# Kernel tuning notes

Hardware: AMD Instinct MI355X
Metric: run time of the kernel (lower is better)

The kernel has to match this reference:

```python
import jax, jax.numpy as jnp
import numpy as np

T, LQ, C = 6, 300, 256
NH, NL, PC, TW, PT = 8, 4, 4, 2, 2
DFF = 1024
HD = C // NH
SHAPES = [(96, 128), (48, 64), (24, 32), (12, 16)]
LIN = sum(h * w for h, w in SHAPES)
EPS = 1e-5


def _ln(x, g, b):
    m = x.mean(-1, keepdims=True)
    v = ((x - m) ** 2).mean(-1, keepdims=True)
    return (x - m) * jax.lax.rsqrt(v + EPS) * g + b


def _bilinear(img, loc):
    # img [T, Hl, Wl, NH, HD]; loc [T, Q, NH, P, 2] (x, y), normalized [0,1],
    # grid_sample align_corners=False + zero padding convention.
    Hl, Wl = img.shape[1], img.shape[2]
    x = loc[..., 0] * Wl - 0.5
    y = loc[..., 1] * Hl - 0.5
    x0f = jnp.floor(x)
    y0f = jnp.floor(y)
    wx = x - x0f
    wy = y - y0f
    x0 = x0f.astype(jnp.int32)
    y0 = y0f.astype(jnp.int32)
    flat = img.transpose(0, 3, 1, 2, 4).reshape(img.shape[0], NH, Hl * Wl, HD)
    b = jnp.arange(img.shape[0])[:, None, None, None]
    h = jnp.arange(NH)[None, :, None, None]

    def corner(yi, xi, w):
        valid = (xi >= 0) & (xi < Wl) & (yi >= 0) & (yi < Hl)
        idx = jnp.clip(yi, 0, Hl - 1) * Wl + jnp.clip(xi, 0, Wl - 1)
        g = flat[b, h, idx.transpose(0, 2, 1, 3)]  # [T, NH, Q, P, HD]
        w = jnp.where(valid, w, 0.0).transpose(0, 2, 1, 3)
        return g * w[..., None]

    out = (corner(y0, x0, (1 - wx) * (1 - wy)) + corner(y0, x0 + 1, wx * (1 - wy))
           + corner(y0 + 1, x0, (1 - wx) * wy) + corner(y0 + 1, x0 + 1, wx * wy))
    return out.transpose(0, 2, 1, 3, 4)  # [T, Q, NH, P, HD]


def _forward(tgt, query_pos, reference_points, curr_frame_offsets,
             other_frames_temporal_offsets, src, src_padding_mask,
             in_proj_w, in_proj_b, sa_out_w, sa_out_b,
             norm1_g, norm1_b, norm2_g, norm2_b, norm3_g, norm3_b,
             value_w, value_b, soff_w, soff_b, toff_w, toff_b,
             attn_w, attn_b, cross_out_w, cross_out_b,
             lin1_w, lin1_b, lin2_w, lin2_b):
    # ---- self attention (per-frame MHA over queries) ----
    q = tgt + query_pos
    wq, wk, wv = jnp.split(in_proj_w, 3, axis=0)
    bq, bk, bv = jnp.split(in_proj_b, 3)
    qh = ((q @ wq.T + bq) * (1.0 / np.sqrt(HD))).reshape(T, LQ, NH, HD)
    kh = (q @ wk.T + bk).reshape(T, LQ, NH, HD)
    vh = (tgt @ wv.T + bv).reshape(T, LQ, NH, HD)
    att = jax.nn.softmax(jnp.einsum('bqhd,bkhd->bhqk', qh, kh), axis=-1)
    sa = jnp.einsum('bhqk,bkhd->bqhd', att, vh).reshape(T, LQ, C) @ sa_out_w.T + sa_out_b
    tgt = _ln(tgt + sa, norm2_g, norm2_b)

    # ---- temporal multi-scale deformable cross attention ----
    qc = tgt + query_pos
    value = src @ value_w.T + value_b
    value = jnp.where(src_padding_mask[..., None], 0.0, value)
    value = value.reshape(T, LIN, NH, HD)

    soff = (qc @ soff_w.T + soff_b).reshape(T, LQ, NH, NL, PC, 2)
    toff = (qc @ toff_w.T + toff_b).reshape(T, LQ, NH, NL, TW, PT, 2)
    aw = (qc @ attn_w.T + attn_b).reshape(T, LQ, NH, NL * (PC + TW * PT))
    aw = jax.nn.softmax(aw, axis=-1).reshape(T, LQ, NH, NL, PC + TW * PT)
    aw_c = aw[..., :PC]                                  # [T,LQ,NH,NL,PC]
    aw_t = aw[..., PC:].reshape(T, LQ, NH, NL, TW, PT)

    norm = jnp.array([[w, h] for h, w in SHAPES], jnp.float32)  # [NL,2] (x,y)
    ref = reference_points[:, :, None, :, None, :]       # [T,LQ,1,NL,1,2]
    cfo = curr_frame_offsets[:, :, None, :, None, :]
    loc_c = ref + cfo + soff / norm[None, None, None, :, None, :]
    ofo = other_frames_temporal_offsets.transpose(0, 1, 3, 2, 4)[:, :, None, :, :, None, :]
    loc_t = ref[:, :, :, :, None, :, :] + ofo + toff / norm[None, None, None, :, None, None, :]

    # temporal window frame indices: nearest neighbours, clipped to clip bounds
    deltas = np.array([-(i // 2 + 1) if i % 2 == 0 else (i // 2 + 1) for i in range(TW)])
    frame_idx = np.clip(np.arange(T)[:, None] + deltas[None, :], 0, T - 1)  # [T,TW]

    out = jnp.zeros((T, LQ, NH, HD), tgt.dtype)
    start = 0
    for l, (hl, wl) in enumerate(SHAPES):
        v_l = value[:, start:start + hl * wl].reshape(T, hl, wl, NH, HD)
        s = _bilinear(v_l, loc_c[:, :, :, l])            # [T,LQ,NH,PC,HD]
        out = out + (s * aw_c[:, :, :, l, :, None]).sum(3)
        for w in range(TW):
            s = _bilinear(v_l[frame_idx[:, w]], loc_t[:, :, :, l, w])
            out = out + (s * aw_t[:, :, :, l, w, :, None]).sum(3)
        start += hl * wl
    cross = out.reshape(T, LQ, C) @ cross_out_w.T + cross_out_b
    tgt = _ln(tgt + cross, norm1_g, norm1_b)

    # ---- FFN ----
    ff = jax.nn.relu(tgt @ lin1_w.T + lin1_b) @ lin2_w.T + lin2_b
    return _ln(tgt + ff, norm3_g, norm3_b)


def setup_inputs():
    ks = jax.random.split(jax.random.key(0), 24)
    r = lambda i, s: jax.random.normal(ks[i], s, jnp.float32)
    u = lambda i, s: jax.random.uniform(ks[i], s, dtype=jnp.float32)
    w = lambda i, s: r(i, s) * 0.02
    shp = np.array(SHAPES, np.int64)
    lsi = np.concatenate([[0], np.cumsum(shp[:, 0] * shp[:, 1])[:-1]])
    return {
        'tgt': r(0, (T, LQ, C)),
        'query_pos': r(1, (T, LQ, C)),
        'reference_points': u(2, (T, LQ, NL, 2)),
        'curr_frame_offsets': u(3, (T, LQ, NL, 2)) * 0.1,
        'other_frames_temporal_offsets': u(4, (T, LQ, TW, NL, 2)) * 0.1,
        'src': r(5, (T, LIN, C)),
        'src_spatial_shapes': jnp.asarray(shp),
        'level_start_index': jnp.asarray(lsi),
        'src_padding_mask': jnp.zeros((T, LIN), bool),
        'in_proj_w': w(6, (3 * C, C)), 'in_proj_b': jnp.zeros((3 * C,)),
        'sa_out_w': w(7, (C, C)), 'sa_out_b': jnp.zeros((C,)),
        'norm1_g': jnp.ones((C,)), 'norm1_b': jnp.zeros((C,)),
        'norm2_g': jnp.ones((C,)), 'norm2_b': jnp.zeros((C,)),
        'norm3_g': jnp.ones((C,)), 'norm3_b': jnp.zeros((C,)),
        'value_w': w(8, (C, C)), 'value_b': jnp.zeros((C,)),
        'soff_w': w(9, (NH * NL * PC * 2, C)), 'soff_b': jnp.zeros((NH * NL * PC * 2,)),
        'toff_w': w(10, (NH * NL * TW * PT * 2, C)), 'toff_b': jnp.zeros((NH * NL * TW * PT * 2,)),
        'attn_w': w(11, (NH * NL * (PC + TW * PT), C)), 'attn_b': jnp.zeros((NH * NL * (PC + TW * PT),)),
        'cross_out_w': w(12, (C, C)), 'cross_out_b': jnp.zeros((C,)),
        'lin1_w': w(13, (DFF, C)), 'lin1_b': jnp.zeros((DFF,)),
        'lin2_w': w(14, (C, DFF)), 'lin2_b': jnp.zeros((C,)),
    }


def reference(tgt, query_pos, reference_points, curr_frame_offsets,
              other_frames_temporal_offsets, src, src_spatial_shapes,
              level_start_index, src_padding_mask,
              in_proj_w, in_proj_b, sa_out_w, sa_out_b,
              norm1_g, norm1_b, norm2_g, norm2_b, norm3_g, norm3_b,
              value_w, value_b, soff_w, soff_b, toff_w, toff_b,
              attn_w, attn_b, cross_out_w, cross_out_b,
              lin1_w, lin1_b, lin2_w, lin2_b):
    # src_spatial_shapes / level_start_index are static (match SHAPES constants)
    return _forward(tgt, query_pos, reference_points, curr_frame_offsets,
                    other_frames_temporal_offsets, src, src_padding_mask,
                    in_proj_w, in_proj_b, sa_out_w, sa_out_b,
                    norm1_g, norm1_b, norm2_g, norm2_b, norm3_g, norm3_b,
                    value_w, value_b, soff_w, soff_b, toff_w, toff_b,
                    attn_w, attn_b, cross_out_w, cross_out_b,
                    lin1_w, lin1_b, lin2_w, lin2_b)
```

## Files before the change

### kernel.cpp

```cpp
#include <hip/hip_runtime.h>
#include <hip/hip_bf16.h>
#include <math.h>

#define T_ 6
#define LQ_ 300
#define C_ 256
#define NH_ 8
#define HD_ 32
#define DFF_ 1024
#define LIN_ 16320
#define NQ_ (T_*LQ_)

typedef unsigned int uint32;
typedef unsigned short us;

__device__ __forceinline__ float b2f(us u) {
    union { float f; unsigned i; } x; x.i = ((unsigned)u) << 16; return x.f;
}
__device__ __forceinline__ us f2b(float f) {
    union { float f; unsigned i; } x; x.f = f;
    unsigned r = x.i + 0x7fffu + ((x.i >> 16) & 1u);
    return (us)(r >> 16);
}
__device__ __forceinline__ uint32 pack2(float a, float b) {
    union { __hip_bfloat162 h; uint32 u; } c;
    c.h = __float22bfloat162_rn(make_float2(a, b));
    return c.u;
}

typedef __bf16 bf16x8 __attribute__((ext_vector_type(8)));
typedef float  f32x4  __attribute__((ext_vector_type(4)));

__device__ __forceinline__ void gemm64_core(
        us* As, us* Bs, int bm,
        const float* __restrict__ A, const float* __restrict__ A2,
        const float* __restrict__ Bw,
        const float* __restrict__ bias, float* __restrict__ Cmat,
        int ldc, int cn0, int M, int K, bool relu) {
    constexpr int LDA = 40;
    int tid  = threadIdx.x;
    int wave = tid >> 6, lane = tid & 63;
    int wm = (wave >> 1) * 32, wn = (wave & 1) * 32;

    f32x4 acc00 = {0.f,0.f,0.f,0.f}, acc01 = {0.f,0.f,0.f,0.f};
    f32x4 acc10 = {0.f,0.f,0.f,0.f}, acc11 = {0.f,0.f,0.f,0.f};

    int srow = tid >> 2, scol = (tid & 3) * 8;
    int arow = bm + srow;
    const bool aval = arow < M;
    const size_t aoff = (size_t)arow * K + scol;
    const size_t boff = (size_t)srow * K + scol;

    int fr = lane & 15, quad = lane >> 4;
    const us* pa0 = As + (wm + fr) * LDA + quad * 8;
    const us* pa1 = pa0 + 16 * LDA;
    const us* pb0 = Bs + (wn + fr) * LDA + quad * 8;
    const us* pb1 = pb0 + 16 * LDA;

    for (int k0 = 0; k0 < K; k0 += 256) {
        float4 ar[8][2], br[8][2];
        #pragma unroll
        for (int c = 0; c < 8; ++c) {
            int kk = k0 + c * 32;
            if (aval) {
                ar[c][0] = *(const float4*)(A + aoff + kk);
                ar[c][1] = *(const float4*)(A + aoff + kk + 4);
                if (A2) {
                    float4 p0 = *(const float4*)(A2 + aoff + kk);
                    float4 p1 = *(const float4*)(A2 + aoff + kk + 4);
                    ar[c][0].x += p0.x; ar[c][0].y += p0.y; ar[c][0].z += p0.z; ar[c][0].w += p0.w;
                    ar[c][1].x += p1.x; ar[c][1].y += p1.y; ar[c][1].z += p1.z; ar[c][1].w += p1.w;
                }
            } else {
                ar[c][0] = make_float4(0.f,0.f,0.f,0.f);
                ar[c][1] = make_float4(0.f,0.f,0.f,0.f);
            }
            br[c][0] = *(const float4*)(Bw + boff + kk);
            br[c][1] = *(const float4*)(Bw + boff + kk + 4);
        }
        #pragma unroll
        for (int c = 0; c < 8; ++c) {
            uint4 ap, bp;
            ap.x = pack2(ar[c][0].x, ar[c][0].y); ap.y = pack2(ar[c][0].z, ar[c][0].w);
            ap.z = pack2(ar[c][1].x, ar[c][1].y); ap.w = pack2(ar[c][1].z, ar[c][1].w);
            bp.x = pack2(br[c][0].x, br[c][0].y); bp.y = pack2(br[c][0].z, br[c][0].w);
            bp.z = pack2(br[c][1].x, br[c][1].y); bp.w = pack2(br[c][1].z, br[c][1].w);
            __syncthreads();
            *(uint4*)(As + srow * LDA + scol) = ap;
            *(uint4*)(Bs + srow * LDA + scol) = bp;
            __syncthreads();
            bf16x8 a0 = *(const bf16x8*)pa0;
            bf16x8 a1 = *(const bf16x8*)pa1;
            bf16x8 b0 = *(const bf16x8*)pb0;
            bf16x8 b1 = *(const bf16x8*)pb1;
            acc00 = __builtin_amdgcn_mfma_f32_16x16x32_bf16(a0, b0, acc00, 0, 0, 0);
            acc01 = __builtin_amdgcn_mfma_f32_16x16x32_bf16(a0, b1, acc01, 0, 0, 0);
            acc10 = __builtin_amdgcn_mfma_f32_16x16x32_bf16(a1, b0, acc10, 0, 0, 0);
            acc11 = __builtin_amdgcn_mfma_f32_16x16x32_bf16(a1, b1, acc11, 0, 0, 0);
        }
    }

    int n0l = wn + fr, n1l = n0l + 16;
    float bias0 = bias[n0l], bias1 = bias[n1l];
    int mbase = bm + wm + quad * 4;
    #pragma unroll
    for (int r = 0; r < 4; ++r) {
        int m0 = mbase + r, m1 = m0 + 16;
        float v00 = acc00[r] + bias0, v01 = acc01[r] + bias1;
        float v10 = acc10[r] + bias0, v11 = acc11[r] + bias1;
        if (relu) {
            v00 = fmaxf(v00, 0.f); v01 = fmaxf(v01, 0.f);
            v10 = fmaxf(v10, 0.f); v11 = fmaxf(v11, 0.f);
        }
        if (m0 < M) {
            Cmat[(size_t)m0 * ldc + cn0 + n0l] = v00;
            Cmat[(size_t)m0 * ldc + cn0 + n1l] = v01;
        }
        if (m1 < M) {
            Cmat[(size_t)m1 * ldc + cn0 + n0l] = v10;
            Cmat[(size_t)m1 * ldc + cn0 + n1l] = v11;
        }
    }
}

template<bool RELU>
__global__ __launch_bounds__(256, 2) void gemm_std(
        const float* __restrict__ A, const float* __restrict__ W,
        const float* __restrict__ bias, float* __restrict__ C,
        int M, int N, int K) {
    __shared__ __align__(16) us As[64 * 40];
    __shared__ __align__(16) us Bs[64 * 40];
    int cn0 = blockIdx.y * 64;
    gemm64_core(As, Bs, blockIdx.x * 64, A, nullptr, W + (size_t)cn0 * K, bias + cn0,
                C, N, cn0, M, K, RELU);
}

__global__ __launch_bounds__(256, 2) void gemm_proj3(
        const float* __restrict__ qc,
        const float* __restrict__ sw, const float* __restrict__ sb,
        const float* __restrict__ tw, const float* __restrict__ tb,
        const float* __restrict__ aw, const float* __restrict__ ab,
        float* __restrict__ so, float* __restrict__ to, float* __restrict__ ao) {
    __shared__ __align__(16) us As[64 * 40];
    __shared__ __align__(16) us Bs[64 * 40];
    int y = blockIdx.y, g = y >> 2, cn0 = (y & 3) * 64;
    const float* W; const float* bias; float* O;
    if (g == 0)      { W = sw; bias = sb; O = so; }
    else if (g == 1) { W = tw; bias = tb; O = to; }
    else             { W = aw; bias = ab; O = ao; }
    gemm64_core(As, Bs, blockIdx.x * 64, qc, nullptr, W + (size_t)cn0 * 256, bias + cn0,
                O, 256, cn0, NQ_, 256, false);
}

__global__ __launch_bounds__(256, 2) void vqkv_kernel(
        const float* __restrict__ src, const float* __restrict__ val_w,
        const float* __restrict__ val_b, us* __restrict__ value,
        const float* __restrict__ tgt, const float* __restrict__ qpos,
        const float* __restrict__ in_w, const float* __restrict__ in_b,
        float* __restrict__ qkb, float* __restrict__ vbuf) {
    __shared__ __align__(16) char smem[32768];
    if (blockIdx.x >= 1530) {
        us* As64 = (us*)smem;
        us* Bs64 = (us*)(smem + 5120);
        int u = blockIdx.x - 1530, y = u / 29, bm = (u % 29) * 64;
        if (y < 8)
            gemm64_core(As64, Bs64, bm, tgt, qpos, in_w + (size_t)y * 64 * 256,
                        in_b + y * 64, qkb, 512, y * 64, NQ_, 256, false);
        else
            gemm64_core(As64, Bs64, bm, tgt, nullptr,
                        in_w + (size_t)(512 + (y - 8) * 64) * 256,
                        in_b + 512 + (y - 8) * 64, vbuf, 256, (y - 8) * 64,
                        NQ_, 256, false);
        return;
    }
    constexpr int LDA = 40;
    us* As = (us*)smem;
    us* Bs = (us*)(smem + 5120);
    int tid = threadIdx.x, wave = tid >> 6, lane = tid & 63;
    int bm = blockIdx.x * 64;
    int fr = lane & 15, quad = lane >> 4;

    f32x4 acc[4][4];
    #pragma unroll
    for (int i = 0; i < 4; ++i)
        #pragma unroll
        for (int j = 0; j < 4; ++j) { f32x4 z = {0.f,0.f,0.f,0.f}; acc[i][j] = z; }

    float4 av[2], bv[8];
    auto ldA = [&](int c) {
        int k0 = c * 32;
        #pragma unroll
        for (int i = 0; i < 2; ++i) {
            int f = i * 256 + tid;
            av[i] = *(const float4*)(src + (size_t)(bm + (f >> 3)) * 256 + k0 + (f & 7) * 4);
        }
    };
    auto ldB = [&](int c) {
        int k0 = c * 32;
        #pragma unroll
        for (int i = 0; i < 8; ++i) {
            int f = i * 256 + tid;
            bv[i] = *(const float4*)(val_w + (size_t)(f >> 3) * 256 + k0 + (f & 7) * 4);
        }
    };

    ldA(0); ldB(0);
    for (int c = 0; c < 8; ++c) {
        if (c) __syncthreads();
        #pragma unroll
        for (int i = 0; i < 2; ++i) {
            int f = i * 256 + tid;
            uint2 p; p.x = pack2(av[i].x, av[i].y); p.y = pack2(av[i].z, av[i].w);
            *(uint2*)(As + (f >> 3) * LDA + (f & 7) * 4) = p;
        }
        #pragma unroll
        for (int i = 0; i < 8; ++i) {
            int f = i * 256 + tid;
            uint2 p; p.x = pack2(bv[i].x, bv[i].y); p.y = pack2(bv[i].z, bv[i].w);
            *(uint2*)(Bs + (f >> 3) * LDA + (f & 7) * 4) = p;
        }
        __syncthreads();
        if (c + 1 < 8) { ldA(c + 1); ldB(c + 1); }
        bf16x8 af[4], bfv[4];
        #pragma unroll
        for (int mt = 0; mt < 4; ++mt)
            af[mt] = *(const bf16x8*)(As + (mt * 16 + fr) * LDA + quad * 8);
        #pragma unroll
        for (int nt = 0; nt < 4; ++nt)
            bfv[nt] = *(const bf16x8*)(Bs + (wave * 64 + nt * 16 + fr) * LDA + quad * 8);
        #pragma unroll
        for (int mt = 0; mt < 4; ++mt)
            #pragma unroll
            for (int nt = 0; nt < 4; ++nt)
                acc[mt][nt] = __builtin_amdgcn_mfma_f32_16x16x32_bf16(af[mt], bfv[nt], acc[mt][nt], 0, 0, 0);
    }

    __syncthreads();
    us* Cs = (us*)smem;
    #pragma unroll
    for (int nt = 0; nt < 4; ++nt) {
        int n = wave * 64 + nt * 16 + fr;
        float bs = val_b[n];
        #pragma unroll
        for (int mt = 0; mt < 4; ++mt) {
            int rowb = mt * 16 + quad * 4;
            #pragma unroll
            for (int r = 0; r < 4; ++r)
                Cs[(rowb + r) * 256 + n] = f2b(acc[mt][nt][r] + bs);
        }
    }
    __syncthreads();
    #pragma unroll
    for (int p = 0; p < 4; ++p) {
        int flat = p * 256 + tid;
        int row = flat >> 5, c16 = (flat & 31) * 8;
        uint4 v = *(const uint4*)(Cs + row * 256 + c16);
        *(uint4*)(value + (size_t)(bm + row) * 256 + c16) = v;
    }
}

__global__ __launch_bounds__(256) void attn_kernel(
        const float* __restrict__ qk, const float* __restrict__ vb,
        float* __restrict__ sain) {
    __shared__ uint32 Ksu[300 * 17];
    __shared__ uint32 Vsu[300 * 17];
    __shared__ float  Qs[32 * 32];
    __shared__ float  ps[4][304];
    int t = blockIdx.x / NH_, h = blockIdx.x % NH_;
    int q0 = blockIdx.y * 32;
    int tid = threadIdx.x;

    for (int idx = tid; idx < 300 * 16; idx += 256) {
        int row = idx >> 4, cc = idx & 15;
        float2 kv = *(const float2*)(qk + (size_t)(t * 300 + row) * 512 + 256 + h * 32 + 2 * cc);
        float2 vv = *(const float2*)(vb + (size_t)(t * 300 + row) * 256 + h * 32 + 2 * cc);
        Ksu[row * 17 + cc] = pack2(kv.x, kv.y);
        Vsu[row * 17 + cc] = pack2(vv.x, vv.y);
    }
    for (int idx = tid; idx < 1024; idx += 256) {
        int row = idx >> 5, d = idx & 31;
        int q = q0 + row;
        Qs[idx] = (q < 300) ? qk[(size_t)(t * 300 + q) * 512 + h * 32 + d] : 0.f;
    }
    __syncthreads();

    int wavei = tid >> 6, lane = tid & 63;
    const float scale = 0.17677669529663687f;

    for (int i = 0; i < 8; ++i) {
        int q = q0 + wavei * 8 + i;
        int ql = wavei * 8 + i;
        float qv[32];
        #pragma unroll
        for (int d = 0; d < 32; ++d) qv[d] = Qs[ql * 32 + d];

        float sc[5], mx = -1e30f;
        #pragma unroll
        for (int m = 0; m < 5; ++m) {
            int k = lane + 64 * m;
            float s = -1e30f;
            if (k < 300) {
                s = 0.f;
                #pragma unroll
                for (int dd = 0; dd < 16; ++dd) {
                    uint32 u = Ksu[k * 17 + dd];
                    s += qv[2 * dd]     * b2f((us)u)
                       + qv[2 * dd + 1] * b2f((us)(u >> 16));
                }
                s *= scale;
            }
            sc[m] = s; mx = fmaxf(mx, s);
        }
        #pragma unroll
        for (int off = 1; off < 64; off <<= 1) mx = fmaxf(mx, __shfl_xor(mx, off));
        float sum = 0.f;
        #pragma unroll
        for (int m = 0; m < 5; ++m) {
            int k = lane + 64 * m;
            float ev = (k < 300) ? __expf(sc[m] - mx) : 0.f;
            if (k < 300) ps[wavei][k] = ev;
            sum += ev;
        }
        #pragma unroll
        for (int off = 1; off < 64; off <<= 1) sum += __shfl_xor(sum, off);
        float inv = 1.f / sum;
        __syncthreads();

        int e16 = lane & 15, kh = lane >> 4;
        float ox = 0.f, oy = 0.f;
        int kbeg = kh * 75;
        for (int k = kbeg; k < kbeg + 75; ++k) {
            float p = ps[wavei][k];
            uint32 u = Vsu[k * 17 + e16];
            ox += p * b2f((us)u);
            oy += p * b2f((us)(u >> 16));
        }
        ox += __shfl_xor(ox, 16); ox += __shfl_xor(ox, 32);
        oy += __shfl_xor(oy, 16); oy += __shfl_xor(oy, 32);
        if (q < 300 && kh == 0) {
            *(float2*)(sain + (size_t)(t * 300 + q) * 256 + h * 32 + 2 * e16)
                = make_float2(ox * inv, oy * inv);
        }
        __syncthreads();
    }
}

__global__ __launch_bounds__(256) void sample_kernel(
        const float* __restrict__ awl,   const float* __restrict__ refp,
        const float* __restrict__ cfo,   const float* __restrict__ ofo,
        const float* __restrict__ soffo, const float* __restrict__ toffo,
        const us* __restrict__ value, float* __restrict__ samp) {
    int b = blockIdx.x;
    int t = b / LQ_;
    int tid = threadIdx.x, h = tid >> 5, d = tid & 31;
    size_t row = (size_t)b;

    float logit = awl[row * 256 + (size_t)tid];
    float mx = logit;
    #pragma unroll
    for (int off = 16; off >= 1; off >>= 1) mx = fmaxf(mx, __shfl_xor(mx, off, 32));
    float e = __expf(logit - mx);
    float s = e;
    #pragma unroll
    for (int off = 16; off >= 1; off >>= 1) s += __shfl_xor(s, off, 32);
    float myw = e / s;

    float soff_my = soffo[row * 256 + (size_t)tid];
    float toff_my = toffo[row * 256 + (size_t)tid];
    float rp_my = (d < 8)  ? refp[row * 8 + d]  : 0.f;
    float cf_my = (d < 8)  ? cfo[row * 8 + d]   : 0.f;
    float of_my = (d < 16) ? ofo[row * 16 + d]  : 0.f;

    float acc = 0.f;
    #pragma unroll
    for (int smp = 0; smp < 32; ++smp) {
        const int l = smp >> 3, j = smp & 7;
        const int Hl = (l == 0) ? 96 : (l == 1) ? 48 : (l == 2) ? 24 : 12;
        const int Wl = (l == 0) ? 128 : (l == 1) ? 64 : (l == 2) ? 32 : 16;
        const int st = (l == 0) ? 0 : (l == 1) ? 12288 : (l == 2) ? 15360 : 16128;
        const float iW = 1.f / (float)Wl, iH = 1.f / (float)Hl;

        float wgt = __shfl(myw, smp, 32);
        float rx = __shfl(rp_my, l * 2 + 0, 32);
        float ry = __shfl(rp_my, l * 2 + 1, 32);
        float lx, ly; int frame;
        if (j < 4) {
            lx = rx + __shfl(cf_my, l * 2 + 0, 32) + __shfl(soff_my, l * 8 + j * 2 + 0, 32) * iW;
            ly = ry + __shfl(cf_my, l * 2 + 1, 32) + __shfl(soff_my, l * 8 + j * 2 + 1, 32) * iH;
            frame = t;
        } else {
            const int wi = (j - 4) >> 1, p = (j - 4) & 1;
            lx = rx + __shfl(of_my, wi * 8 + l * 2 + 0, 32) + __shfl(toff_my, l * 8 + wi * 4 + p * 2 + 0, 32) * iW;
            ly = ry + __shfl(of_my, wi * 8 + l * 2 + 1, 32) + __shfl(toff_my, l * 8 + wi * 4 + p * 2 + 1, 32) * iH;
            frame = t + (wi == 0 ? -1 : 1);
            frame = frame < 0 ? 0 : (frame > T_ - 1 ? T_ - 1 : frame);
        }
        float x = lx * (float)Wl - 0.5f, y = ly * (float)Hl - 0.5f;
        float xf = floorf(x), yf = floorf(y);
        float wx = x - xf, wy = y - yf;
        int x0 = (int)xf, y0 = (int)yf;
        int x1 = x0 + 1, y1 = y0 + 1;
        float vx0 = (x0 >= 0 && x0 < Wl) ? 1.f : 0.f;
        float vx1 = (x1 >= 0 && x1 < Wl) ? 1.f : 0.f;
        float vy0 = (y0 >= 0 && y0 < Hl) ? 1.f : 0.f;
        float vy1 = (y1 >= 0 && y1 < Hl) ? 1.f : 0.f;
        int cx0 = min(max(x0, 0), Wl - 1), cx1 = min(max(x1, 0), Wl - 1);
        int cy0 = min(max(y0, 0), Hl - 1), cy1 = min(max(y1, 0), Hl - 1);
        size_t base = ((size_t)frame * LIN_ + st) * 256 + h * 32 + d;
        float g00 = b2f(value[base + (size_t)(cy0 * Wl + cx0) * 256]);
        float g01 = b2f(value[base + (size_t)(cy0 * Wl + cx1) * 256]);
        float g10 = b2f(value[base + (size_t)(cy1 * Wl + cx0) * 256]);
        float g11 = b2f(value[base + (size_t)(cy1 * Wl + cx1) * 256]);
        float w00 = (1.f - wx) * (1.f - wy) * vx0 * vy0;
        float w01 = wx * (1.f - wy) * vx1 * vy0;
        float w10 = (1.f - wx) * wy * vx0 * vy1;
        float w11 = wx * wy * vx1 * vy1;
        acc += wgt * (g00 * w00 + g01 * w01 + g10 * w10 + g11 * w11);
    }
    samp[row * 256 + (size_t)tid] = acc;
}

__global__ __launch_bounds__(256) void ln_kernel(
        const float* __restrict__ x, const float* __restrict__ y,
        const float* __restrict__ g, const float* __restrict__ bb,
        float* __restrict__ out,
        const float* __restrict__ pos, float* __restrict__ out2) {
    int row = blockIdx.x, c = threadIdx.x;
    size_t idx = (size_t)row * 256 + c;
    float v = x[idx] + y[idx];
    float s = v;
    #pragma unroll
    for (int off = 1; off < 64; off <<= 1) s += __shfl_xor(s, off);
    __shared__ float red[4];
    int wv = c >> 6;
    if ((c & 63) == 0) red[wv] = s;
    __syncthreads();
    float mean = (red[0] + red[1] + red[2] + red[3]) * (1.0f / 256.0f);
    float dv = v - mean;
    float s2 = dv * dv;
    #pragma unroll
    for (int off = 1; off < 64; off <<= 1) s2 += __shfl_xor(s2, off);
    __syncthreads();
    if ((c & 63) == 0) red[wv] = s2;
    __syncthreads();
    float var = (red[0] + red[1] + red[2] + red[3]) * (1.0f / 256.0f);
    float o = dv * rsqrtf(var + 1e-5f) * g[c] + bb[c];
    out[idx] = o;
    if (out2) out2[idx] = o + pos[idx];
}

extern "C" void kernel_launch(void* const* d_in, const int* in_sizes, int n_in,
                              void* d_out, int out_size, void* d_ws, size_t ws_size,
                              hipStream_t stream) {
    (void)in_sizes; (void)n_in; (void)out_size; (void)ws_size;
    typedef const float* cfp;
    cfp tgt   = (cfp)d_in[0];
    cfp qpos  = (cfp)d_in[1];
    cfp refp  = (cfp)d_in[2];
    cfp cfo   = (cfp)d_in[3];
    cfp ofo   = (cfp)d_in[4];
    cfp src   = (cfp)d_in[5];
    cfp in_proj_w = (cfp)d_in[9];
    cfp in_proj_b = (cfp)d_in[10];
    cfp sa_out_w  = (cfp)d_in[11];
    cfp sa_out_b  = (cfp)d_in[12];
    cfp n1g = (cfp)d_in[13], n1b = (cfp)d_in[14];
    cfp n2g = (cfp)d_in[15], n2b = (cfp)d_in[16];
    cfp n3g = (cfp)d_in[17], n3b = (cfp)d_in[18];
    cfp value_w = (cfp)d_in[19], value_b = (cfp)d_in[20];
    cfp soff_w = (cfp)d_in[21], soff_b = (cfp)d_in[22];
    cfp toff_w = (cfp)d_in[23], toff_b = (cfp)d_in[24];
    cfp attn_w = (cfp)d_in[25], attn_b = (cfp)d_in[26];
    cfp cross_w = (cfp)d_in[27], cross_b = (cfp)d_in[28];
    cfp lin1_w = (cfp)d_in[29], lin1_b = (cfp)d_in[30];
    cfp lin2_w = (cfp)d_in[31], lin2_b = (cfp)d_in[32];

    char* wp = (char*)d_ws;
    const size_t ROWB = (size_t)NQ_ * 256 * 4;
    us* value = (us*)wp;  wp += (size_t)T_ * LIN_ * 256 * 2;
    float* bigreg = (float*)wp;  wp += 4 * ROWB;
    float* qkb  = bigreg;
    float* vbuf = bigreg + (size_t)NQ_ * 512;
    float* ff1  = bigreg;
    float* sain   = (float*)wp; wp += ROWB;   float* awl    = sain;
    float* sap    = (float*)wp; wp += ROWB;   float* soffo  = sap;
    float* tgt2   = (float*)wp; wp += ROWB;   float* ff2    = tgt2;
    float* qc     = (float*)wp; wp += ROWB;   float* samp   = qc;
    float* toffo  = (float*)wp; wp += ROWB;
    float* crossp = (float*)wp; wp += ROWB;
    float* tgt3   = (float*)wp; wp += ROWB;

    dim3 blk(256);
    const int mb = (NQ_ + 63) / 64;

    vqkv_kernel<<<dim3(1530 + 348), blk, 0, stream>>>(
        src, value_w, value_b, value, tgt, qpos, in_proj_w, in_proj_b, qkb, vbuf);
    attn_kernel<<<dim3(T_ * NH_, 10), blk, 0, stream>>>(qkb, vbuf, sain);
    gemm_std<false><<<dim3(mb, 4), blk, 0, stream>>>(sain, sa_out_w, sa_out_b, sap, NQ_, 256, 256);
    ln_kernel<<<dim3(NQ_), blk, 0, stream>>>(tgt, sap, n2g, n2b, tgt2, qpos, qc);
    gemm_proj3<<<dim3(mb, 12), blk, 0, stream>>>(qc, soff_w, soff_b, toff_w, toff_b,
                                                 attn_w, attn_b, soffo, toffo, awl);
    sample_kernel<<<dim3(NQ_), blk, 0, stream>>>(awl, refp, cfo, ofo, soffo, toffo, value, samp);
    gemm_std<false><<<dim3(mb, 4), blk, 0, stream>>>(samp, cross_w, cross_b, crossp, NQ_, 256, 256);
    ln_kernel<<<dim3(NQ_), blk, 0, stream>>>(tgt2, crossp, n1g, n1b, tgt3, nullptr, nullptr);
    gemm_std<true><<<dim3(mb, 16), blk, 0, stream>>>(tgt3, lin1_w, lin1_b, ff1, NQ_, 1024, 256);
    gemm_std<false><<<dim3(mb, 4), blk, 0, stream>>>(ff1, lin2_w, lin2_b, ff2, NQ_, 256, 1024);
    ln_kernel<<<dim3(NQ_), blk, 0, stream>>>(tgt3, ff2, n3g, n3b, (float*)d_out, nullptr, nullptr);
}
```

Before: 374.1 us.

## Fuse output GEMMs with residual LayerNorm and cross projection into sampling

Adds a 16-row-tile MFMA GEMM kernel that applies bias, the residual add and LayerNorm in its epilogue. It replaces the self-attention output and FFN second GEMM, each of which was followed by a separate LN kernel. The cross-attention output projection now runs as a per-row matrix-vector product inside the sampling kernel, followed by LN1. Its weight is pre-transposed to bf16 by an extra block in the first kernel. This removes several launches and intermediate round trips through global memory. In exchange, every sampling block now streams the full 256x256 bf16 weight from cache with scalar FMAs, and LN variance is computed as E[x²]−mean² in the fused GEMM kernel. The value store loop is also widened to cover all 64 tile rows.

```diff
diff --git a/kernel.cpp b/kernel.cpp
--- a/kernel.cpp
+++ b/kernel.cpp
@@ -157,12 +157,20 @@
         const float* __restrict__ val_b, us* __restrict__ value,
         const float* __restrict__ tgt, const float* __restrict__ qpos,
         const float* __restrict__ in_w, const float* __restrict__ in_b,
-        float* __restrict__ qkb, float* __restrict__ vbuf) {
+        float* __restrict__ qkb, float* __restrict__ vbuf,
+        const float* __restrict__ cross_w, us* __restrict__ wck) {
     __shared__ __align__(16) char smem[32768];
-    if (blockIdx.x >= 1530) {
+    int tid = threadIdx.x;
+    if (blockIdx.x == 0) {
+        int n = tid;
+        for (int k = 0; k < 256; ++k)
+            wck[(size_t)k * 256 + n] = f2b(cross_w[(size_t)n * 256 + k]);
+        return;
+    }
+    if (blockIdx.x >= 1531) {
         us* As64 = (us*)smem;
         us* Bs64 = (us*)(smem + 5120);
-        int u = blockIdx.x - 1530, y = u / 29, bm = (u % 29) * 64;
+        int u = blockIdx.x - 1531, y = u / 29, bm = (u % 29) * 64;
         if (y < 8)
             gemm64_core(As64, Bs64, bm, tgt, qpos, in_w + (size_t)y * 64 * 256,
                         in_b + y * 64, qkb, 512, y * 64, NQ_, 256, false);
@@ -176,8 +184,8 @@
     constexpr int LDA = 40;
     us* As = (us*)smem;
     us* Bs = (us*)(smem + 5120);
-    int tid = threadIdx.x, wave = tid >> 6, lane = tid & 63;
-    int bm = blockIdx.x * 64;
+    int wave = tid >> 6, lane = tid & 63;
+    int bm = (blockIdx.x - 1) * 64;
     int fr = lane & 15, quad = lane >> 4;
 
     f32x4 acc[4][4];
@@ -251,11 +259,125 @@
     }
     __syncthreads();
     #pragma unroll
-    for (int p = 0; p < 4; ++p) {
+    for (int p = 0; p < 8; ++p) {
         int flat = p * 256 + tid;
         int row = flat >> 5, c16 = (flat & 31) * 8;
         uint4 v = *(const uint4*)(Cs + row * 256 + c16);
         *(uint4*)(value + (size_t)(bm + row) * 256 + c16) = v;
+    }
+}
+
+__global__ __launch_bounds__(256, 3) void gemmln16(
+        const float* __restrict__ A, const float* __restrict__ W,
+        const float* __restrict__ bias, int M, int K,
+        const float* __restrict__ resid, const float* __restrict__ lng,
+        const float* __restrict__ lnb, float* __restrict__ out_ln,
+        const float* __restrict__ pos, float* __restrict__ out2) {
+    constexpr int LDA = 40;
+    __shared__ __align__(16) us As[16 * 40];
+    __shared__ __align__(16) us Bs[256 * 40];
+    __shared__ float lred[2][16][4];
+    __shared__ float lmv[2][16];
+    int tid = threadIdx.x, wave = tid >> 6, lane = tid & 63;
+    int fr = lane & 15, quad = lane >> 4;
+    int bm = blockIdx.x * 16;
+
+    f32x4 acc[4];
+    #pragma unroll
+    for (int nt = 0; nt < 4; ++nt) { f32x4 z = {0.f,0.f,0.f,0.f}; acc[nt] = z; }
+
+    const int KC = K >> 5;
+    float4 av, bv[8];
+    auto ldA = [&](int c) {
+        if (tid < 128) {
+            int r = bm + (tid >> 3);
+            if (r < M) av = *(const float4*)(A + (size_t)r * K + c * 32 + (tid & 7) * 4);
+            else       av = make_float4(0.f, 0.f, 0.f, 0.f);
+        }
+    };
+    auto ldB = [&](int c) {
+        int k0 = c * 32;
+        #pragma unroll
+        for (int i = 0; i < 8; ++i) {
+            int f = i * 256 + tid;
+            bv[i] = *(const float4*)(W + (size_t)(f >> 3) * K + k0 + (f & 7) * 4);
+        }
+    };
+
+    ldA(0); ldB(0);
+    for (int c = 0; c < KC; ++c) {
+        if (c) __syncthreads();
+        if (tid < 128) {
+            uint2 p; p.x = pack2(av.x, av.y); p.y = pack2(av.z, av.w);
+            *(uint2*)(As + (tid >> 3) * LDA + (tid & 7) * 4) = p;
+        }
+        #pragma unroll
+        for (int i = 0; i < 8; ++i) {
+            int f = i * 256 + tid;
+            uint2 p; p.x = pack2(bv[i].x, bv[i].y); p.y = pack2(bv[i].z, bv[i].w);
+            *(uint2*)(Bs + (f >> 3) * LDA + (f & 7) * 4) = p;
+        }
+        __syncthreads();
+        if (c + 1 < KC) { ldA(c + 1); ldB(c + 1); }
+        bf16x8 af = *(const bf16x8*)(As + fr * LDA + quad * 8);
+        #pragma unroll
+        for (int nt = 0; nt < 4; ++nt) {
+            bf16x8 bf = *(const bf16x8*)(Bs + (wave * 64 + nt * 16 + fr) * LDA + quad * 8);
+            acc[nt] = __builtin_amdgcn_mfma_f32_16x16x32_bf16(af, bf, acc[nt], 0, 0, 0);
+        }
+    }
+
+    int col[4]; float bcol[4];
+    #pragma unroll
+    for (int nt = 0; nt < 4; ++nt) { col[nt] = wave * 64 + nt * 16 + fr; bcol[nt] = bias[col[nt]]; }
+    #pragma unroll
+    for (int r = 0; r < 4; ++r) {
+        int m = bm + quad * 4 + r;
+        #pragma unroll
+        for (int nt = 0; nt < 4; ++nt) {
+            float rv = (m < M) ? resid[(size_t)m * 256 + col[nt]] : 0.f;
+            acc[nt][r] += bcol[nt] + rv;
+        }
+    }
+    #pragma unroll
+    for (int r = 0; r < 4; ++r) {
+        float s  = acc[0][r] + acc[1][r] + acc[2][r] + acc[3][r];
+        float s2 = acc[0][r]*acc[0][r] + acc[1][r]*acc[1][r]
+                 + acc[2][r]*acc[2][r] + acc[3][r]*acc[3][r];
+        #pragma unroll
+        for (int off = 1; off < 16; off <<= 1) {
+            s  += __shfl_xor(s,  off);
+            s2 += __shfl_xor(s2, off);
+        }
+        if (fr == 0) {
+            lred[0][quad * 4 + r][wave] = s;
+            lred[1][quad * 4 + r][wave] = s2;
+        }
+    }
+    __syncthreads();
+    if (tid < 16) {
+        float s  = lred[0][tid][0] + lred[0][tid][1] + lred[0][tid][2] + lred[0][tid][3];
+        float s2 = lred[1][tid][0] + lred[1][tid][1] + lred[1][tid][2] + lred[1][tid][3];
+        float mean = s * (1.0f / 256.0f);
+        float var  = s2 * (1.0f / 256.0f) - mean * mean;
+        lmv[0][tid] = mean;
+        lmv[1][tid] = rsqrtf(var + 1e-5f);
+    }
+    __syncthreads();
+    float gcol[4], b2col[4];
+    #pragma unroll
+    for (int nt = 0; nt < 4; ++nt) { gcol[nt] = lng[col[nt]]; b2col[nt] = lnb[col[nt]]; }
+    #pragma unroll
+    for (int r = 0; r < 4; ++r) {
+        int row16 = quad * 4 + r, m = bm + row16;
+        if (m >= M) continue;
+        float mean = lmv[0][row16], rstd = lmv[1][row16];
+        #pragma unroll
+        for (int nt = 0; nt < 4; ++nt) {
+            float o = (acc[nt][r] - mean) * rstd * gcol[nt] + b2col[nt];
+            out_ln[(size_t)m * 256 + col[nt]] = o;
+            if (pos) out2[(size_t)m * 256 + col[nt]] = o + pos[(size_t)m * 256 + col[nt]];
+        }
     }
 }
 
@@ -345,11 +467,16 @@
     }
 }
 
-__global__ __launch_bounds__(256) void sample_kernel(
+__global__ __launch_bounds__(256) void scln_kernel(
         const float* __restrict__ awl,   const float* __restrict__ refp,
         const float* __restrict__ cfo,   const float* __restrict__ ofo,
         const float* __restrict__ soffo, const float* __restrict__ toffo,
-        const us* __restrict__ value, float* __restrict__ samp) {
+        const us* __restrict__ value,    const us* __restrict__ wck,
+        const float* __restrict__ cross_b, const float* __restrict__ tgt2,
+        const float* __restrict__ n1g,   const float* __restrict__ n1b,
+        float* __restrict__ tgt3) {
+    __shared__ float srow[256];
+    __shared__ float red[4];
     int b = blockIdx.x;
     int t = b / LQ_;
     int tid = threadIdx.x, h = tid >> 5, d = tid & 31;
@@ -417,23 +544,23 @@
         float w11 = wx * wy * vx1 * vy1;
         acc += wgt * (g00 * w00 + g01 * w01 + g10 * w10 + g11 * w11);
     }
-    samp[row * 256 + (size_t)tid] = acc;
-}
-
-__global__ __launch_bounds__(256) void ln_kernel(
-        const float* __restrict__ x, const float* __restrict__ y,
-        const float* __restrict__ g, const float* __restrict__ bb,
-        float* __restrict__ out,
-        const float* __restrict__ pos, float* __restrict__ out2) {
-    int row = blockIdx.x, c = threadIdx.x;
-    size_t idx = (size_t)row * 256 + c;
-    float v = x[idx] + y[idx];
-    float s = v;
-    #pragma unroll
-    for (int off = 1; off < 64; off <<= 1) s += __shfl_xor(s, off);
-    __shared__ float red[4];
-    int wv = c >> 6;
-    if ((c & 63) == 0) red[wv] = s;
+    srow[tid] = acc;
+    __syncthreads();
+
+    float cv = cross_b[tid];
+    #pragma unroll 2
+    for (int k0 = 0; k0 < 256; k0 += 8) {
+        #pragma unroll
+        for (int j = 0; j < 8; ++j)
+            cv += srow[k0 + j] * b2f(wck[(size_t)(k0 + j) * 256 + tid]);
+    }
+    float v = cv + tgt2[row * 256 + tid];
+
+    float sm = v;
+    #pragma unroll
+    for (int off = 1; off < 64; off <<= 1) sm += __shfl_xor(sm, off);
+    int wv = tid >> 6;
+    if ((tid & 63) == 0) red[wv] = sm;
     __syncthreads();
     float mean = (red[0] + red[1] + red[2] + red[3]) * (1.0f / 256.0f);
     float dv = v - mean;
@@ -441,12 +568,10 @@
     #pragma unroll
     for (int off = 1; off < 64; off <<= 1) s2 += __shfl_xor(s2, off);
     __syncthreads();
-    if ((c & 63) == 0) red[wv] = s2;
+    if ((tid & 63) == 0) red[wv] = s2;
     __syncthreads();
     float var = (red[0] + red[1] + red[2] + red[3]) * (1.0f / 256.0f);
-    float o = dv * rsqrtf(var + 1e-5f) * g[c] + bb[c];
-    out[idx] = o;
-    if (out2) out2[idx] = o + pos[idx];
+    tgt3[row * 256 + tid] = dv * rsqrtf(var + 1e-5f) * n1g[tid] + n1b[tid];
 }
 
 extern "C" void kernel_launch(void* const* d_in, const int* in_sizes, int n_in,
@@ -482,28 +607,29 @@
     float* qkb  = bigreg;
     float* vbuf = bigreg + (size_t)NQ_ * 512;
     float* ff1  = bigreg;
-    float* sain   = (float*)wp; wp += ROWB;   float* awl    = sain;
-    float* sap    = (float*)wp; wp += ROWB;   float* soffo  = sap;
-    float* tgt2   = (float*)wp; wp += ROWB;   float* ff2    = tgt2;
-    float* qc     = (float*)wp; wp += ROWB;   float* samp   = qc;
+    float* sain   = (float*)wp; wp += ROWB;   float* awl = sain;
+    float* soffo  = (float*)wp; wp += ROWB;
+    float* tgt2   = (float*)wp; wp += ROWB;
+    float* qc     = (float*)wp; wp += ROWB;
     float* toffo  = (float*)wp; wp += ROWB;
-    float* crossp = (float*)wp; wp += ROWB;
     float* tgt3   = (float*)wp; wp += ROWB;
+    us* wck       = (us*)wp;    wp += 256 * 256 * 2;
 
     dim3 blk(256);
     const int mb = (NQ_ + 63) / 64;
-
-    vqkv_kernel<<<dim3(1530 + 348), blk, 0, stream>>>(
-        src, value_w, value_b, value, tgt, qpos, in_proj_w, in_proj_b, qkb, vbuf);
+    const int mb16 = (NQ_ + 15) / 16;
+
+    vqkv_kernel<<<dim3(1879), blk, 0, stream>>>(
+        src, value_w, value_b, value, tgt, qpos, in_proj_w, in_proj_b, qkb, vbuf,
+        cross_w, wck);
     attn_kernel<<<dim3(T_ * NH_, 10), blk, 0, stream>>>(qkb, vbuf, sain);
-    gemm_std<false><<<dim3(mb, 4), blk, 0, stream>>>(sain, sa_out_w, sa_out_b, sap, NQ_, 256, 256);
-    ln_kernel<<<dim3(NQ_), blk, 0, stream>>>(tgt, sap, n2g, n2b, tgt2, qpos, qc);
+    gemmln16<<<dim3(mb16), blk, 0, stream>>>(
+        sain, sa_out_w, sa_out_b, NQ_, 256, tgt, n2g, n2b, tgt2, qpos, qc);
     gemm_proj3<<<dim3(mb, 12), blk, 0, stream>>>(qc, soff_w, soff_b, toff_w, toff_b,
                                                  attn_w, attn_b, soffo, toffo, awl);
-    sample_kernel<<<dim3(NQ_), blk, 0, stream>>>(awl, refp, cfo, ofo, soffo, toffo, value, samp);
-    gemm_std<false><<<dim3(mb, 4), blk, 0, stream>>>(samp, cross_w, cross_b, crossp, NQ_, 256, 256);
-    ln_kernel<<<dim3(NQ_), blk, 0, stream>>>(tgt2, crossp, n1g, n1b, tgt3, nullptr, nullptr);
+    scln_kernel<<<dim3(NQ_), blk, 0, stream>>>(awl, refp, cfo, ofo, soffo, toffo,
+                                               value, wck, cross_b, tgt2, n1g, n1b, tgt3);
     gemm_std<true><<<dim3(mb, 16), blk, 0, stream>>>(tgt3, lin1_w, lin1_b, ff1, NQ_, 1024, 256);
-    gemm_std<false><<<dim3(mb, 4), blk, 0, stream>>>(ff1, lin2_w, lin2_b, ff2, NQ_, 256, 1024);
-    ln_kernel<<<dim3(NQ_), blk, 0, stream>>>(tgt3, ff2, n3g, n3b, (float*)d_out, nullptr, nullptr);
-}
+    gemmln16<<<dim3(mb16), blk, 0, stream>>>(
+        ff1, lin2_w, lin2_b, NQ_, 1024, tgt3, n3g, n3b, (float*)d_out, nullptr, nullptr);
+}
```

New measurement: 388.8 us. 3.9% more time.
